# Performance work log

Hardware: AMD Instinct MI355X
Metric: run time of the kernel (lower is better)

Reference implementation:

```python
import jax, jax.numpy as jnp
import numpy as np

N = 10000      # nodes
E = 640000     # directed edges
D = 128        # feature width
C = 10         # classes
G = 64         # graphs in batch


def setup_inputs() -> dict:
    key = jax.random.key(0)
    ks = jax.random.split(key, 9)
    x = jax.random.normal(ks[0], (N, D), dtype=jnp.float32)
    edge_index = jax.random.randint(ks[1], (2, E), 0, N, dtype=jnp.int64)
    batch = jnp.sort(jax.random.randint(ks[2], (N,), 0, G, dtype=jnp.int64))
    scale = 1.0 / np.sqrt(D)
    W1 = jax.random.normal(ks[3], (D, D), dtype=jnp.float32) * scale
    W2 = jax.random.normal(ks[4], (D, D), dtype=jnp.float32) * scale
    W3 = jax.random.normal(ks[5], (D, D), dtype=jnp.float32) * scale
    W4 = jax.random.normal(ks[6], (D, D), dtype=jnp.float32) * scale
    fc_w = jax.random.normal(ks[7], (D, C), dtype=jnp.float32) * scale
    fc_b = jnp.zeros((C,), dtype=jnp.float32)
    return {"x": x, "edge_index": edge_index, "batch": batch,
            "W1": W1, "W2": W2, "W3": W3, "W4": W4,
            "fc_w": fc_w, "fc_b": fc_b}


def _gcn_conv(x, src, dst, deg_inv_sqrt, W):
    # GCNConv: h = x @ W; aggregate D^{-1/2}(A+I)D^{-1/2} h; then ReLU (activation).
    h = x @ W                                        # [N, D]
    norm = deg_inv_sqrt[src] * deg_inv_sqrt[dst]     # [E]
    msgs = h[src] * norm[:, None]                    # gather + scale
    agg = jax.ops.segment_sum(msgs, dst, num_segments=N)
    agg = agg + h * (deg_inv_sqrt * deg_inv_sqrt)[:, None]  # self-loop term
    return jax.nn.relu(agg)


def reference(x, edge_index, batch, W1, W2, W3, W4, fc_w, fc_b):
    src, dst = edge_index[0], edge_index[1]
    # degree counting self-loops (A + I normalization)
    deg = jax.ops.segment_sum(jnp.ones((E,), x.dtype), dst, num_segments=N) + 1.0
    deg_inv_sqrt = jax.lax.rsqrt(deg)
    for W in (W1, W2, W3, W4):
        x = _gcn_conv(x, src, dst, deg_inv_sqrt, W)
    xr = jax.ops.segment_sum(x, batch, num_segments=G)   # global_add_pool
    logits = x @ fc_w + fc_b
    return jax.nn.log_softmax(logits, axis=1), xr
```

## Files before the change

### kernel.cpp

```cpp
#include <hip/hip_runtime.h>
#include <hip/hip_fp16.h>
#include <math.h>

#define N_NODES 10000
#define N_EDGES 640000
#define DIM     128
#define NCLS    10
#define NGRAPH  64
#define NB      157
#define BCAP    4608
#define EPB     4000
#define NPB     8

typedef unsigned int uint32;
typedef unsigned short ushort16;
typedef _Float16 h2v __attribute__((ext_vector_type(2)));

#define SEL_LO 0x00003C00u
#define SEL_HI 0x3C000000u

__device__ __forceinline__ h2v as_h2(uint32 u) { h2v r; __builtin_memcpy(&r, &u, 4); return r; }

__device__ __forceinline__ float fd2(uint32 w, uint32 p, float acc) {
#if __has_builtin(__builtin_amdgcn_fdot2)
    return __builtin_amdgcn_fdot2(as_h2(w), as_h2(p), acc, false);
#else
    h2v a = as_h2(w), b = as_h2(p);
    return acc + (float)a[0] * (float)b[0] + (float)a[1] * (float)b[1];
#endif
}
__device__ __forceinline__ float f16lo(uint32 u) { return (float)as_h2(u)[0]; }
__device__ __forceinline__ float f16hi(uint32 u) { return (float)as_h2(u)[1]; }
__device__ __forceinline__ ushort16 f32_f16(float f) {
    return __half_as_ushort(__float2half(f));
}
__device__ __forceinline__ uint32 pack_f16x2(float lo, float hi) {
    __half2 h = __floats2half2_rn(lo, hi);
    uint32 u; __builtin_memcpy(&u, &h, 4); return u;
}

__global__ __launch_bounds__(256) void binA_gemm1(const int* __restrict__ src,
                                                  const int* __restrict__ dst,
                                                  int* __restrict__ gcursor,
                                                  uint32* __restrict__ bins,
                                                  const float* __restrict__ X,
                                                  const float* __restrict__ W,
                                                  const float* __restrict__ W2,
                                                  const float* __restrict__ W3,
                                                  const float* __restrict__ W4,
                                                  uint32* __restrict__ Wp,
                                                  ushort16* __restrict__ Gh,
                                                  float* __restrict__ xr) {
    __shared__ uint32 pk[EPB];
    __shared__ int cntS[NB], offS[NB], curS[NB], gposS[NB];

    if (blockIdx.x < 625) {
        int c    = threadIdx.x & 127;
        int rg   = threadIdx.x >> 7;
        int row0 = blockIdx.x * 16 + rg * 8;
        const float* xb = X + row0 * DIM;
        float acc[8] = {0.f, 0.f, 0.f, 0.f, 0.f, 0.f, 0.f, 0.f};
        for (int k = 0; k < DIM; k += 4) {
            float w0 = W[(k + 0) * DIM + c];
            float w1 = W[(k + 1) * DIM + c];
            float w2 = W[(k + 2) * DIM + c];
            float w3 = W[(k + 3) * DIM + c];
#pragma unroll
            for (int r = 0; r < 8; r++) {
                float4 xv = *(const float4*)(xb + r * DIM + k);
                acc[r] += xv.x * w0 + xv.y * w1 + xv.z * w2 + xv.w * w3;
            }
        }
#pragma unroll
        for (int r = 0; r < 8; r++)
            Gh[(row0 + r) * DIM + c] = f32_f16(acc[r]);
        return;
    }

    if (blockIdx.x >= 786) {
        int w = blockIdx.x - 786;
        const float* Ws = (w == 0) ? W2 : (w == 1) ? W3 : W4;
        uint32* Wd = Wp + w * (64 * DIM);
        for (int i = threadIdx.x; i < 64 * DIM; i += 256) {
            int k2 = i >> 7, c = i & 127;
            Wd[i] = pack_f16x2(Ws[(2 * k2) * DIM + c], Ws[(2 * k2 + 1) * DIM + c]);
        }
        return;
    }

    if (blockIdx.x == 785) {
        float4 z = make_float4(0.f, 0.f, 0.f, 0.f);
        for (int j = threadIdx.x; j < NGRAPH * DIM / 4; j += 256)
            ((float4*)xr)[j] = z;
        return;
    }

    int ab  = blockIdx.x - 625;
    int tid = threadIdx.x;
    for (int i = tid; i < NB; i += 256) cntS[i] = 0;
    __syncthreads();

    int base = ab * EPB;
    uint32 pr[16];
#pragma unroll
    for (int it = 0; it < 16; it++) {
        int i = it * 256 + tid;
        uint32 p = 0xffffffffu;
        if (i < EPB) {
            int e = base + i;
            p = ((uint32)dst[e] << 16) | (uint32)src[e];
            atomicAdd(&cntS[p >> 22], 1);
        }
        pr[it] = p;
    }
    __syncthreads();

    if (tid < 64) {
        int carry = 0;
        for (int r = 0; r < 3; r++) {
            int idx = r * 64 + tid;
            int v = (idx < NB) ? cntS[idx] : 0;
            int inc = v;
#pragma unroll
            for (int o = 1; o < 64; o <<= 1) {
                int u = __shfl_up(inc, o, 64);
                if (tid >= o) inc += u;
            }
            if (idx < NB) { offS[idx] = inc - v + carry; curS[idx] = inc - v + carry; }
            carry += __shfl(inc, 63, 64);
        }
    }
    __syncthreads();

#pragma unroll
    for (int it = 0; it < 16; it++) {
        uint32 p = pr[it];
        if (p != 0xffffffffu) {
            int b = p >> 22;
            pk[atomicAdd(&curS[b], 1)] = p;
        }
    }
    __syncthreads();

    if (tid < NB) gposS[tid] = atomicAdd(&gcursor[tid], cntS[tid]);
    __syncthreads();

#pragma unroll
    for (int it = 0; it < 16; it++) {
        int i = it * 256 + tid;
        if (i < EPB) {
            uint32 u = pk[i];
            int b = u >> 22;
            int gp = gposS[b] + (i - offS[b]);
            if (gp < BCAP) bins[b * BCAP + gp] = u;
        }
    }
}

__global__ __launch_bounds__(256) void binB2(const int* __restrict__ gcursor,
                                             const uint32* __restrict__ bins,
                                             ushort16* __restrict__ col,
                                             int* __restrict__ deg,
                                             float* __restrict__ dis,
                                             uint32* __restrict__ disPh) {
    __shared__ ushort16 adj[32 * 128];
    __shared__ int cnt2[32];
    int b    = blockIdx.x >> 1;
    int half = blockIdx.x & 1;
    int tid  = threadIdx.x;
    if (tid < 32) cnt2[tid] = 0;
    __syncthreads();
    int tc = gcursor[b];
    if (tc > BCAP) tc = BCAP;
    const uint32* bb = bins + b * BCAP;
    for (int i = tid; i < tc; i += 256) {
        uint32 u = bb[i];
        int local = (u >> 16) & 63;
        if ((local >> 5) == half) {
            int l5 = local & 31;
            int r = atomicAdd(&cnt2[l5], 1);
            if (r < 128) adj[(l5 << 7) + r] = (ushort16)(u & 0xffffu);
        }
    }
    __syncthreads();
    uint4* dstp = (uint4*)(col + (size_t)b * 64 * 128 + half * 32 * 128);
    const uint4* srcp = (const uint4*)adj;
    for (int j = tid; j < 512; j += 256) dstp[j] = srcp[j];
    if (tid < 32) {
        int node = b * 64 + half * 32 + tid;
        int c = cnt2[tid] < 128 ? cnt2[tid] : 128;
        float dv = rsqrtf((float)c + 1.0f);
        deg[node] = c;
        dis[node] = dv;
        disPh[node] = (uint32)__half_as_ushort(__float2half(dv));
    }
}

template <bool SCALED_IN, bool PACK_OUT>
__device__ __forceinline__ void agg_to_lds(const ushort16* __restrict__ Gh,
                                           const int* __restrict__ deg,
                                           const ushort16* __restrict__ col,
                                           const float* __restrict__ dis,
                                           const uint32* __restrict__ disPh,
                                           void* __restrict__ Xout) {
    int tid  = threadIdx.x;
    int wave = tid >> 6;
    int lane = tid & 63;
    int grp  = lane >> 4;
    int sl   = lane & 15;
    const uint32* g32 = (const uint32*)Gh;
    const uint32* gp  = g32 + (sl << 2);

#pragma unroll
    for (int i = 0; i < 2; i++) {
        int vr = wave * 2 + i;
        int v  = blockIdx.x * NPB + vr;
        int dv = deg[v];
        uint32 colpack = ((const uint32*)(col + ((size_t)v << 7)))[lane];
        float acc[8];
#pragma unroll
        for (int j = 0; j < 8; j++) acc[j] = 0.f;

        int kk = 0;
        for (; kk + 16 <= dv; kk += 16) {
            int k0 = kk + grp, k1 = kk + 4 + grp, k2 = kk + 8 + grp, k3 = kk + 12 + grp;
            uint32 cp0 = __shfl(colpack, k0 >> 1, 64);
            uint32 cp1 = __shfl(colpack, k1 >> 1, 64);
            uint32 cp2 = __shfl(colpack, k2 >> 1, 64);
            uint32 cp3 = __shfl(colpack, k3 >> 1, 64);
            int u0 = (k0 & 1) ? (int)(cp0 >> 16) : (int)(cp0 & 0xffffu);
            int u1 = (k1 & 1) ? (int)(cp1 >> 16) : (int)(cp1 & 0xffffu);
            int u2 = (k2 & 1) ? (int)(cp2 >> 16) : (int)(cp2 & 0xffffu);
            int u3 = (k3 & 1) ? (int)(cp3 >> 16) : (int)(cp3 & 0xffffu);
            uint4 w0 = *(const uint4*)(gp + (u0 << 6));
            uint4 w1 = *(const uint4*)(gp + (u1 << 6));
            uint4 w2 = *(const uint4*)(gp + (u2 << 6));
            uint4 w3 = *(const uint4*)(gp + (u3 << 6));
            if (SCALED_IN) {
                acc[0] = fd2(w0.x, SEL_LO, acc[0]); acc[1] = fd2(w0.x, SEL_HI, acc[1]);
                acc[2] = fd2(w0.y, SEL_LO, acc[2]); acc[3] = fd2(w0.y, SEL_HI, acc[3]);
                acc[4] = fd2(w0.z, SEL_LO, acc[4]); acc[5] = fd2(w0.z, SEL_HI, acc[5]);
                acc[6] = fd2(w0.w, SEL_LO, acc[6]); acc[7] = fd2(w0.w, SEL_HI, acc[7]);
                acc[0] = fd2(w1.x, SEL_LO, acc[0]); acc[1] = fd2(w1.x, SEL_HI, acc[1]);
                acc[2] = fd2(w1.y, SEL_LO, acc[2]); acc[3] = fd2(w1.y, SEL_HI, acc[3]);
                acc[4] = fd2(w1.z, SEL_LO, acc[4]); acc[5] = fd2(w1.z, SEL_HI, acc[5]);
                acc[6] = fd2(w1.w, SEL_LO, acc[6]); acc[7] = fd2(w1.w, SEL_HI, acc[7]);
                acc[0] = fd2(w2.x, SEL_LO, acc[0]); acc[1] = fd2(w2.x, SEL_HI, acc[1]);
                acc[2] = fd2(w2.y, SEL_LO, acc[2]); acc[3] = fd2(w2.y, SEL_HI, acc[3]);
                acc[4] = fd2(w2.z, SEL_LO, acc[4]); acc[5] = fd2(w2.z, SEL_HI, acc[5]);
                acc[6] = fd2(w2.w, SEL_LO, acc[6]); acc[7] = fd2(w2.w, SEL_HI, acc[7]);
                acc[0] = fd2(w3.x, SEL_LO, acc[0]); acc[1] = fd2(w3.x, SEL_HI, acc[1]);
                acc[2] = fd2(w3.y, SEL_LO, acc[2]); acc[3] = fd2(w3.y, SEL_HI, acc[3]);
                acc[4] = fd2(w3.z, SEL_LO, acc[4]); acc[5] = fd2(w3.z, SEL_HI, acc[5]);
                acc[6] = fd2(w3.w, SEL_LO, acc[6]); acc[7] = fd2(w3.w, SEL_HI, acc[7]);
            } else {
                uint32 dp0 = disPh[u0], dp1 = disPh[u1], dp2 = disPh[u2], dp3 = disPh[u3];
                uint32 dq0 = dp0 << 16, dq1 = dp1 << 16, dq2 = dp2 << 16, dq3 = dp3 << 16;
                acc[0] = fd2(w0.x, dp0, acc[0]); acc[1] = fd2(w0.x, dq0, acc[1]);
                acc[2] = fd2(w0.y, dp0, acc[2]); acc[3] = fd2(w0.y, dq0, acc[3]);
                acc[4] = fd2(w0.z, dp0, acc[4]); acc[5] = fd2(w0.z, dq0, acc[5]);
                acc[6] = fd2(w0.w, dp0, acc[6]); acc[7] = fd2(w0.w, dq0, acc[7]);
                acc[0] = fd2(w1.x, dp1, acc[0]); acc[1] = fd2(w1.x, dq1, acc[1]);
                acc[2] = fd2(w1.y, dp1, acc[2]); acc[3] = fd2(w1.y, dq1, acc[3]);
                acc[4] = fd2(w1.z, dp1, acc[4]); acc[5] = fd2(w1.z, dq1, acc[5]);
                acc[6] = fd2(w1.w, dp1, acc[6]); acc[7] = fd2(w1.w, dq1, acc[7]);
                acc[0] = fd2(w2.x, dp2, acc[0]); acc[1] = fd2(w2.x, dq2, acc[1]);
                acc[2] = fd2(w2.y, dp2, acc[2]); acc[3] = fd2(w2.y, dq2, acc[3]);
                acc[4] = fd2(w2.z, dp2, acc[4]); acc[5] = fd2(w2.z, dq2, acc[5]);
                acc[6] = fd2(w2.w, dp2, acc[6]); acc[7] = fd2(w2.w, dq2, acc[7]);
                acc[0] = fd2(w3.x, dp3, acc[0]); acc[1] = fd2(w3.x, dq3, acc[1]);
                acc[2] = fd2(w3.y, dp3, acc[2]); acc[3] = fd2(w3.y, dq3, acc[3]);
                acc[4] = fd2(w3.z, dp3, acc[4]); acc[5] = fd2(w3.z, dq3, acc[5]);
                acc[6] = fd2(w3.w, dp3, acc[6]); acc[7] = fd2(w3.w, dq3, acc[7]);
            }
        }
        for (; kk + 8 <= dv; kk += 8) {
            int k0 = kk + grp, k1 = kk + 4 + grp;
            uint32 cp0 = __shfl(colpack, k0 >> 1, 64);
            uint32 cp1 = __shfl(colpack, k1 >> 1, 64);
            int u0 = (k0 & 1) ? (int)(cp0 >> 16) : (int)(cp0 & 0xffffu);
            int u1 = (k1 & 1) ? (int)(cp1 >> 16) : (int)(cp1 & 0xffffu);
            uint4 w0 = *(const uint4*)(gp + (u0 << 6));
            uint4 w1 = *(const uint4*)(gp + (u1 << 6));
            uint32 dp0 = SCALED_IN ? SEL_LO : disPh[u0];
            uint32 dp1 = SCALED_IN ? SEL_LO : disPh[u1];
            uint32 dq0 = SCALED_IN ? SEL_HI : (dp0 << 16);
            uint32 dq1 = SCALED_IN ? SEL_HI : (dp1 << 16);
            acc[0] = fd2(w0.x, dp0, acc[0]); acc[1] = fd2(w0.x, dq0, acc[1]);
            acc[2] = fd2(w0.y, dp0, acc[2]); acc[3] = fd2(w0.y, dq0, acc[3]);
            acc[4] = fd2(w0.z, dp0, acc[4]); acc[5] = fd2(w0.z, dq0, acc[5]);
            acc[6] = fd2(w0.w, dp0, acc[6]); acc[7] = fd2(w0.w, dq0, acc[7]);
            acc[0] = fd2(w1.x, dp1, acc[0]); acc[1] = fd2(w1.x, dq1, acc[1]);
            acc[2] = fd2(w1.y, dp1, acc[2]); acc[3] = fd2(w1.y, dq1, acc[3]);
            acc[4] = fd2(w1.z, dp1, acc[4]); acc[5] = fd2(w1.z, dq1, acc[5]);
            acc[6] = fd2(w1.w, dp1, acc[6]); acc[7] = fd2(w1.w, dq1, acc[7]);
        }
        for (; kk < dv; kk += 4) {
            int k = kk + grp;
            uint32 cp = __shfl(colpack, (k >> 1) & 63, 64);
            int u = (k & 1) ? (int)(cp >> 16) : (int)(cp & 0xffffu);
            if (k < dv) {
                uint4 w = *(const uint4*)(gp + (u << 6));
                uint32 dp = SCALED_IN ? SEL_LO : disPh[u];
                uint32 dq = SCALED_IN ? SEL_HI : (dp << 16);
                acc[0] = fd2(w.x, dp, acc[0]); acc[1] = fd2(w.x, dq, acc[1]);
                acc[2] = fd2(w.y, dp, acc[2]); acc[3] = fd2(w.y, dq, acc[3]);
                acc[4] = fd2(w.z, dp, acc[4]); acc[5] = fd2(w.z, dq, acc[5]);
                acc[6] = fd2(w.w, dp, acc[6]); acc[7] = fd2(w.w, dq, acc[7]);
            }
        }
#pragma unroll
        for (int j = 0; j < 8; j++) {
            acc[j] += __shfl_xor(acc[j], 16, 64);
            acc[j] += __shfl_xor(acc[j], 32, 64);
        }
        float sv = dis[v];
        uint4 hs = *(const uint4*)(gp + (v << 6));
        float fs = SCALED_IN ? 1.f : sv;
        float r0 = sv * (acc[0] + fs * f16lo(hs.x));
        float r1 = sv * (acc[1] + fs * f16hi(hs.x));
        float r2 = sv * (acc[2] + fs * f16lo(hs.y));
        float r3 = sv * (acc[3] + fs * f16hi(hs.y));
        float r4 = sv * (acc[4] + fs * f16lo(hs.z));
        float r5 = sv * (acc[5] + fs * f16hi(hs.z));
        float r6 = sv * (acc[6] + fs * f16lo(hs.w));
        float r7 = sv * (acc[7] + fs * f16hi(hs.w));
        if (grp == 0) {
            if (PACK_OUT) {
                uint32* o = (uint32*)Xout + vr * 64 + sl * 4;
                uint4 pk4;
                pk4.x = pack_f16x2(fmaxf(r0, 0.f), fmaxf(r1, 0.f));
                pk4.y = pack_f16x2(fmaxf(r2, 0.f), fmaxf(r3, 0.f));
                pk4.z = pack_f16x2(fmaxf(r4, 0.f), fmaxf(r5, 0.f));
                pk4.w = pack_f16x2(fmaxf(r6, 0.f), fmaxf(r7, 0.f));
                *(uint4*)o = pk4;
            } else {
                float4* o = (float4*)((float*)Xout + vr * DIM + sl * 8);
                o[0] = make_float4(fmaxf(r0, 0.f), fmaxf(r1, 0.f),
                                   fmaxf(r2, 0.f), fmaxf(r3, 0.f));
                o[1] = make_float4(fmaxf(r4, 0.f), fmaxf(r5, 0.f),
                                   fmaxf(r6, 0.f), fmaxf(r7, 0.f));
            }
        }
    }
}

template <bool SCALED_IN>
__global__ __launch_bounds__(256) void fused_layer(const ushort16* __restrict__ Gh_in,
                                                   const int* __restrict__ deg,
                                                   const ushort16* __restrict__ col,
                                                   const float* __restrict__ dis,
                                                   const uint32* __restrict__ disPh,
                                                   const uint32* __restrict__ Wp,
                                                   ushort16* __restrict__ Gh_out) {
    __shared__ __align__(16) uint32 Xh[NPB * 64];
    agg_to_lds<SCALED_IN, true>(Gh_in, deg, col, dis, disPh, Xh);
    __syncthreads();

    int c  = threadIdx.x & 127;
    int rg = threadIdx.x >> 7;
    int row0 = blockIdx.x * NPB + rg * 4;
    const uint4* Xh4 = (const uint4*)Xh;
    float acc[4] = {0.f, 0.f, 0.f, 0.f};
    for (int q = 0; q < 16; q++) {
        uint32 wp0 = Wp[(4 * q + 0) * DIM + c];
        uint32 wp1 = Wp[(4 * q + 1) * DIM + c];
        uint32 wp2 = Wp[(4 * q + 2) * DIM + c];
        uint32 wp3 = Wp[(4 * q + 3) * DIM + c];
#pragma unroll
        for (int r = 0; r < 4; r++) {
            uint4 xv = Xh4[(rg * 4 + r) * 16 + q];
            acc[r] = fd2(xv.x, wp0, acc[r]);
            acc[r] = fd2(xv.y, wp1, acc[r]);
            acc[r] = fd2(xv.z, wp2, acc[r]);
            acc[r] = fd2(xv.w, wp3, acc[r]);
        }
    }
#pragma unroll
    for (int r = 0; r < 4; r++) {
        int row = row0 + r;
        Gh_out[row * DIM + c] = f32_f16(acc[r] * dis[row]);
    }
}

__global__ __launch_bounds__(256) void fused_last(const ushort16* __restrict__ Gh_in,
                                                  const int* __restrict__ deg,
                                                  const ushort16* __restrict__ col,
                                                  const float* __restrict__ dis,
                                                  const uint32* __restrict__ disPh,
                                                  const int* __restrict__ batch,
                                                  const float* __restrict__ fcw,
                                                  const float* __restrict__ fcb,
                                                  float* __restrict__ xr,
                                                  float* __restrict__ out) {
    __shared__ float Xs[NPB * DIM];
    agg_to_lds<true, false>(Gh_in, deg, col, dis, disPh, Xs);
    __syncthreads();

    int wave = threadIdx.x >> 6;
    int lane = threadIdx.x & 63;
#pragma unroll
    for (int i = 0; i < 2; i++) {
        int vr   = wave * 2 + i;
        int node = blockIdx.x * NPB + vr;
        float xl = Xs[vr * DIM + lane];
        float xh = Xs[vr * DIM + 64 + lane];
        float lg[NCLS];
#pragma unroll
        for (int c2 = 0; c2 < NCLS; c2++) {
            float p = xl * fcw[lane * NCLS + c2] + xh * fcw[(lane + 64) * NCLS + c2];
#pragma unroll
            for (int off = 32; off >= 1; off >>= 1) p += __shfl_xor(p, off, 64);
            lg[c2] = p + fcb[c2];
        }
        float m = lg[0];
#pragma unroll
        for (int c2 = 1; c2 < NCLS; c2++) m = fmaxf(m, lg[c2]);
        float s = 0.f;
#pragma unroll
        for (int c2 = 0; c2 < NCLS; c2++) s += expf(lg[c2] - m);
        float lse = m + logf(s);
        if (lane < NCLS) out[node * NCLS + lane] = lg[lane] - lse;
    }

    if (threadIdx.x < 128) {
        int start = blockIdx.x * NPB;
        int t = threadIdx.x;
        int b = batch[start];
        float a = 0.f;
        for (int n = 0; n < NPB; n++) {
            int bn = batch[start + n];
            if (bn != b) { atomicAdd(&xr[b * DIM + t], a); a = 0.f; b = bn; }
            a += Xs[n * DIM + t];
        }
        atomicAdd(&xr[b * DIM + t], a);
    }
}


extern "C" void kernel_launch(void* const* d_in, const int* in_sizes, int n_in,
                              void* d_out, int out_size, void* d_ws, size_t ws_size,
                              hipStream_t stream) {
    const float* x     = (const float*)d_in[0];
    const int*   ei    = (const int*)d_in[1];
    const int*   src   = ei;
    const int*   dst   = ei + N_EDGES;
    const int*   batch = (const int*)d_in[2];
    const float* W1    = (const float*)d_in[3];
    const float* W2    = (const float*)d_in[4];
    const float* W3    = (const float*)d_in[5];
    const float* W4    = (const float*)d_in[6];
    const float* fcw   = (const float*)d_in[7];
    const float* fcb   = (const float*)d_in[8];

    float* out_ls = (float*)d_out;
    float* out_xr = out_ls + N_NODES * NCLS;

    int*      gcursor = (int*)d_ws;
    int*      deg     = gcursor + 256;
    float*    dis     = (float*)(deg + 10240);
    uint32*   bins    = (uint32*)(dis + 10240);
    ushort16* col     = (ushort16*)(bins + NB * BCAP);
    ushort16* Gh_a    = col + (size_t)NB * 64 * 128;
    ushort16* Gh_b    = Gh_a + (size_t)N_NODES * DIM;
    uint32*   Wp      = (uint32*)(Gh_b + (size_t)N_NODES * DIM);
    uint32*   disPh   = Wp + 3 * 64 * DIM;

    hipMemsetAsync(gcursor, 0, 256 * sizeof(int), stream);

    binA_gemm1<<<789, 256, 0, stream>>>(src, dst, gcursor, bins, x, W1,
                                        W2, W3, W4, Wp, Gh_a, out_xr);
    binB2     <<<2 * NB, 256, 0, stream>>>(gcursor, bins, col, deg, dis, disPh);

    fused_layer<false><<<N_NODES / NPB, 256, 0, stream>>>(Gh_a, deg, col, dis, disPh,
                                                          Wp, Gh_b);
    fused_layer<true> <<<N_NODES / NPB, 256, 0, stream>>>(Gh_b, deg, col, dis, disPh,
                                                          Wp + 64 * DIM, Gh_a);
    fused_layer<true> <<<N_NODES / NPB, 256, 0, stream>>>(Gh_a, deg, col, dis, disPh,
                                                          Wp + 2 * 64 * DIM, Gh_b);
    fused_last        <<<N_NODES / NPB, 256, 0, stream>>>(Gh_b, deg, col, dis, disPh,
                                                          batch, fcw, fcb, out_xr, out_ls);
}
```

Before: 182.2 us.

## Use fixed per-block bin segments and prescale first-layer features in binB2

Binning now writes each edge block's per-bucket entries into a fixed 64-slot segment with a per-segment count, instead of reserving space with global atomics on a cursor. This removes the memset and the cross-block atomic contention. binB2 also prescales the first layer's fp16 features by the source degree factor, so all layers share one aggregation path with no per-edge disPh gather. The cost is that binB2 scans a sparse 160x64 segment grid, and any segment holding more than 64 entries is silently truncated. That is unlikely with ~25 entries per segment on random inputs, but it is a correctness risk for skewed graphs.

New measurement: 190.4 us. 1.05x slower.

```diff
diff --git a/kernel.cpp b/kernel.cpp
--- a/kernel.cpp
+++ b/kernel.cpp
@@ -8,7 +8,8 @@
 #define NCLS    10
 #define NGRAPH  64
 #define NB      157
-#define BCAP    4608
+#define NBB     160
+#define SEG     64
 #define EPB     4000
 #define NPB     8
 
@@ -41,7 +42,7 @@
 
 __global__ __launch_bounds__(256) void binA_gemm1(const int* __restrict__ src,
                                                   const int* __restrict__ dst,
-                                                  int* __restrict__ gcursor,
+                                                  int* __restrict__ cntG,
                                                   uint32* __restrict__ bins,
                                                   const float* __restrict__ X,
                                                   const float* __restrict__ W,
@@ -52,7 +53,7 @@
                                                   ushort16* __restrict__ Gh,
                                                   float* __restrict__ xr) {
     __shared__ uint32 pk[EPB];
-    __shared__ int cntS[NB], offS[NB], curS[NB], gposS[NB];
+    __shared__ int cntS[NB], offS[NB], curS[NB];
 
     if (blockIdx.x < 625) {
         int c    = threadIdx.x & 127;
@@ -142,66 +143,84 @@
     }
     __syncthreads();
 
-    if (tid < NB) gposS[tid] = atomicAdd(&gcursor[tid], cntS[tid]);
-    __syncthreads();
-
 #pragma unroll
     for (int it = 0; it < 16; it++) {
         int i = it * 256 + tid;
         if (i < EPB) {
             uint32 u = pk[i];
             int b = u >> 22;
-            int gp = gposS[b] + (i - offS[b]);
-            if (gp < BCAP) bins[b * BCAP + gp] = u;
-        }
-    }
-}
-
-__global__ __launch_bounds__(256) void binB2(const int* __restrict__ gcursor,
+            int gp = i - offS[b];
+            if (gp < SEG) bins[(size_t)(b * NBB + ab) * SEG + gp] = u;
+        }
+    }
+    if (tid < NB) {
+        int c = cntS[tid];
+        cntG[tid * NBB + ab] = c < SEG ? c : SEG;
+    }
+}
+
+__global__ __launch_bounds__(256) void binB2(const int* __restrict__ cntG,
                                              const uint32* __restrict__ bins,
                                              ushort16* __restrict__ col,
                                              int* __restrict__ deg,
                                              float* __restrict__ dis,
-                                             uint32* __restrict__ disPh) {
+                                             ushort16* __restrict__ Gh) {
     __shared__ ushort16 adj[32 * 128];
     __shared__ int cnt2[32];
+    __shared__ int segc[NBB];
     int b    = blockIdx.x >> 1;
     int half = blockIdx.x & 1;
     int tid  = threadIdx.x;
     if (tid < 32) cnt2[tid] = 0;
-    __syncthreads();
-    int tc = gcursor[b];
-    if (tc > BCAP) tc = BCAP;
-    const uint32* bb = bins + b * BCAP;
-    for (int i = tid; i < tc; i += 256) {
-        uint32 u = bb[i];
-        int local = (u >> 16) & 63;
-        if ((local >> 5) == half) {
-            int l5 = local & 31;
-            int r = atomicAdd(&cnt2[l5], 1);
-            if (r < 128) adj[(l5 << 7) + r] = (ushort16)(u & 0xffffu);
-        }
-    }
-    __syncthreads();
+    if (tid < NBB) segc[tid] = cntG[b * NBB + tid];
+    __syncthreads();
+
+    const uint32* bb = bins + (size_t)b * NBB * SEG;
+    for (int i = tid; i < NBB * SEG; i += 256) {
+        int seg = i >> 6, idx = i & 63;
+        if (idx < segc[seg]) {
+            uint32 u = bb[i];
+            int local = (u >> 16) & 63;
+            if ((local >> 5) == half) {
+                int l5 = local & 31;
+                int r = atomicAdd(&cnt2[l5], 1);
+                if (r < 128) adj[(l5 << 7) + r] = (ushort16)(u & 0xffffu);
+            }
+        }
+    }
+    __syncthreads();
+
     uint4* dstp = (uint4*)(col + (size_t)b * 64 * 128 + half * 32 * 128);
     const uint4* srcp = (const uint4*)adj;
     for (int j = tid; j < 512; j += 256) dstp[j] = srcp[j];
     if (tid < 32) {
         int node = b * 64 + half * 32 + tid;
         int c = cnt2[tid] < 128 ? cnt2[tid] : 128;
+        deg[node] = c;
+        dis[node] = rsqrtf((float)c + 1.0f);
+    }
+
+    uint4* Gh4 = (uint4*)Gh;
+    int node0 = b * 64 + half * 32;
+    for (int j = tid; j < 32 * 16; j += 256) {
+        int rl = j >> 4, q = j & 15;
+        if (node0 + rl >= N_NODES) continue;
+        int c = cnt2[rl] < 128 ? cnt2[rl] : 128;
         float dv = rsqrtf((float)c + 1.0f);
-        deg[node] = c;
-        dis[node] = dv;
-        disPh[node] = (uint32)__half_as_ushort(__float2half(dv));
-    }
-}
-
-template <bool SCALED_IN, bool PACK_OUT>
+        uint4 g = Gh4[(size_t)(node0 + rl) * 16 + q];
+        g.x = pack_f16x2(f16lo(g.x) * dv, f16hi(g.x) * dv);
+        g.y = pack_f16x2(f16lo(g.y) * dv, f16hi(g.y) * dv);
+        g.z = pack_f16x2(f16lo(g.z) * dv, f16hi(g.z) * dv);
+        g.w = pack_f16x2(f16lo(g.w) * dv, f16hi(g.w) * dv);
+        Gh4[(size_t)(node0 + rl) * 16 + q] = g;
+    }
+}
+
+template <bool PACK_OUT>
 __device__ __forceinline__ void agg_to_lds(const ushort16* __restrict__ Gh,
                                            const int* __restrict__ deg,
                                            const ushort16* __restrict__ col,
                                            const float* __restrict__ dis,
-                                           const uint32* __restrict__ disPh,
                                            void* __restrict__ Xout) {
     int tid  = threadIdx.x;
     int wave = tid >> 6;
@@ -236,43 +255,22 @@
             uint4 w1 = *(const uint4*)(gp + (u1 << 6));
             uint4 w2 = *(const uint4*)(gp + (u2 << 6));
             uint4 w3 = *(const uint4*)(gp + (u3 << 6));
-            if (SCALED_IN) {
-                acc[0] = fd2(w0.x, SEL_LO, acc[0]); acc[1] = fd2(w0.x, SEL_HI, acc[1]);
-                acc[2] = fd2(w0.y, SEL_LO, acc[2]); acc[3] = fd2(w0.y, SEL_HI, acc[3]);
-                acc[4] = fd2(w0.z, SEL_LO, acc[4]); acc[5] = fd2(w0.z, SEL_HI, acc[5]);
-                acc[6] = fd2(w0.w, SEL_LO, acc[6]); acc[7] = fd2(w0.w, SEL_HI, acc[7]);
-                acc[0] = fd2(w1.x, SEL_LO, acc[0]); acc[1] = fd2(w1.x, SEL_HI, acc[1]);
-                acc[2] = fd2(w1.y, SEL_LO, acc[2]); acc[3] = fd2(w1.y, SEL_HI, acc[3]);
-                acc[4] = fd2(w1.z, SEL_LO, acc[4]); acc[5] = fd2(w1.z, SEL_HI, acc[5]);
-                acc[6] = fd2(w1.w, SEL_LO, acc[6]); acc[7] = fd2(w1.w, SEL_HI, acc[7]);
-                acc[0] = fd2(w2.x, SEL_LO, acc[0]); acc[1] = fd2(w2.x, SEL_HI, acc[1]);
-                acc[2] = fd2(w2.y, SEL_LO, acc[2]); acc[3] = fd2(w2.y, SEL_HI, acc[3]);
-                acc[4] = fd2(w2.z, SEL_LO, acc[4]); acc[5] = fd2(w2.z, SEL_HI, acc[5]);
-                acc[6] = fd2(w2.w, SEL_LO, acc[6]); acc[7] = fd2(w2.w, SEL_HI, acc[7]);
-                acc[0] = fd2(w3.x, SEL_LO, acc[0]); acc[1] = fd2(w3.x, SEL_HI, acc[1]);
-                acc[2] = fd2(w3.y, SEL_LO, acc[2]); acc[3] = fd2(w3.y, SEL_HI, acc[3]);
-                acc[4] = fd2(w3.z, SEL_LO, acc[4]); acc[5] = fd2(w3.z, SEL_HI, acc[5]);
-                acc[6] = fd2(w3.w, SEL_LO, acc[6]); acc[7] = fd2(w3.w, SEL_HI, acc[7]);
-            } else {
-                uint32 dp0 = disPh[u0], dp1 = disPh[u1], dp2 = disPh[u2], dp3 = disPh[u3];
-                uint32 dq0 = dp0 << 16, dq1 = dp1 << 16, dq2 = dp2 << 16, dq3 = dp3 << 16;
-                acc[0] = fd2(w0.x, dp0, acc[0]); acc[1] = fd2(w0.x, dq0, acc[1]);
-                acc[2] = fd2(w0.y, dp0, acc[2]); acc[3] = fd2(w0.y, dq0, acc[3]);
-                acc[4] = fd2(w0.z, dp0, acc[4]); acc[5] = fd2(w0.z, dq0, acc[5]);
-                acc[6] = fd2(w0.w, dp0, acc[6]); acc[7] = fd2(w0.w, dq0, acc[7]);
-                acc[0] = fd2(w1.x, dp1, acc[0]); acc[1] = fd2(w1.x, dq1, acc[1]);
-                acc[2] = fd2(w1.y, dp1, acc[2]); acc[3] = fd2(w1.y, dq1, acc[3]);
-                acc[4] = fd2(w1.z, dp1, acc[4]); acc[5] = fd2(w1.z, dq1, acc[5]);
-                acc[6] = fd2(w1.w, dp1, acc[6]); acc[7] = fd2(w1.w, dq1, acc[7]);
-                acc[0] = fd2(w2.x, dp2, acc[0]); acc[1] = fd2(w2.x, dq2, acc[1]);
-                acc[2] = fd2(w2.y, dp2, acc[2]); acc[3] = fd2(w2.y, dq2, acc[3]);
-                acc[4] = fd2(w2.z, dp2, acc[4]); acc[5] = fd2(w2.z, dq2, acc[5]);
-                acc[6] = fd2(w2.w, dp2, acc[6]); acc[7] = fd2(w2.w, dq2, acc[7]);
-                acc[0] = fd2(w3.x, dp3, acc[0]); acc[1] = fd2(w3.x, dq3, acc[1]);
-                acc[2] = fd2(w3.y, dp3, acc[2]); acc[3] = fd2(w3.y, dq3, acc[3]);
-                acc[4] = fd2(w3.z, dp3, acc[4]); acc[5] = fd2(w3.z, dq3, acc[5]);
-                acc[6] = fd2(w3.w, dp3, acc[6]); acc[7] = fd2(w3.w, dq3, acc[7]);
-            }
+            acc[0] = fd2(w0.x, SEL_LO, acc[0]); acc[1] = fd2(w0.x, SEL_HI, acc[1]);
+            acc[2] = fd2(w0.y, SEL_LO, acc[2]); acc[3] = fd2(w0.y, SEL_HI, acc[3]);
+            acc[4] = fd2(w0.z, SEL_LO, acc[4]); acc[5] = fd2(w0.z, SEL_HI, acc[5]);
+            acc[6] = fd2(w0.w, SEL_LO, acc[6]); acc[7] = fd2(w0.w, SEL_HI, acc[7]);
+            acc[0] = fd2(w1.x, SEL_LO, acc[0]); acc[1] = fd2(w1.x, SEL_HI, acc[1]);
+            acc[2] = fd2(w1.y, SEL_LO, acc[2]); acc[3] = fd2(w1.y, SEL_HI, acc[3]);
+            acc[4] = fd2(w1.z, SEL_LO, acc[4]); acc[5] = fd2(w1.z, SEL_HI, acc[5]);
+            acc[6] = fd2(w1.w, SEL_LO, acc[6]); acc[7] = fd2(w1.w, SEL_HI, acc[7]);
+            acc[0] = fd2(w2.x, SEL_LO, acc[0]); acc[1] = fd2(w2.x, SEL_HI, acc[1]);
+            acc[2] = fd2(w2.y, SEL_LO, acc[2]); acc[3] = fd2(w2.y, SEL_HI, acc[3]);
+            acc[4] = fd2(w2.z, SEL_LO, acc[4]); acc[5] = fd2(w2.z, SEL_HI, acc[5]);
+            acc[6] = fd2(w2.w, SEL_LO, acc[6]); acc[7] = fd2(w2.w, SEL_HI, acc[7]);
+            acc[0] = fd2(w3.x, SEL_LO, acc[0]); acc[1] = fd2(w3.x, SEL_HI, acc[1]);
+            acc[2] = fd2(w3.y, SEL_LO, acc[2]); acc[3] = fd2(w3.y, SEL_HI, acc[3]);
+            acc[4] = fd2(w3.z, SEL_LO, acc[4]); acc[5] = fd2(w3.z, SEL_HI, acc[5]);
+            acc[6] = fd2(w3.w, SEL_LO, acc[6]); acc[7] = fd2(w3.w, SEL_HI, acc[7]);
         }
         for (; kk + 8 <= dv; kk += 8) {
             int k0 = kk + grp, k1 = kk + 4 + grp;
@@ -282,18 +280,14 @@
             int u1 = (k1 & 1) ? (int)(cp1 >> 16) : (int)(cp1 & 0xffffu);
             uint4 w0 = *(const uint4*)(gp + (u0 << 6));
             uint4 w1 = *(const uint4*)(gp + (u1 << 6));
-            uint32 dp0 = SCALED_IN ? SEL_LO : disPh[u0];
-            uint32 dp1 = SCALED_IN ? SEL_LO : disPh[u1];
-            uint32 dq0 = SCALED_IN ? SEL_HI : (dp0 << 16);
-            uint32 dq1 = SCALED_IN ? SEL_HI : (dp1 << 16);
-            acc[0] = fd2(w0.x, dp0, acc[0]); acc[1] = fd2(w0.x, dq0, acc[1]);
-            acc[2] = fd2(w0.y, dp0, acc[2]); acc[3] = fd2(w0.y, dq0, acc[3]);
-            acc[4] = fd2(w0.z, dp0, acc[4]); acc[5] = fd2(w0.z, dq0, acc[5]);
-            acc[6] = fd2(w0.w, dp0, acc[6]); acc[7] = fd2(w0.w, dq0, acc[7]);
-            acc[0] = fd2(w1.x, dp1, acc[0]); acc[1] = fd2(w1.x, dq1, acc[1]);
-            acc[2] = fd2(w1.y, dp1, acc[2]); acc[3] = fd2(w1.y, dq1, acc[3]);
-            acc[4] = fd2(w1.z, dp1, acc[4]); acc[5] = fd2(w1.z, dq1, acc[5]);
-            acc[6] = fd2(w1.w, dp1, acc[6]); acc[7] = fd2(w1.w, dq1, acc[7]);
+            acc[0] = fd2(w0.x, SEL_LO, acc[0]); acc[1] = fd2(w0.x, SEL_HI, acc[1]);
+            acc[2] = fd2(w0.y, SEL_LO, acc[2]); acc[3] = fd2(w0.y, SEL_HI, acc[3]);
+            acc[4] = fd2(w0.z, SEL_LO, acc[4]); acc[5] = fd2(w0.z, SEL_HI, acc[5]);
+            acc[6] = fd2(w0.w, SEL_LO, acc[6]); acc[7] = fd2(w0.w, SEL_HI, acc[7]);
+            acc[0] = fd2(w1.x, SEL_LO, acc[0]); acc[1] = fd2(w1.x, SEL_HI, acc[1]);
+            acc[2] = fd2(w1.y, SEL_LO, acc[2]); acc[3] = fd2(w1.y, SEL_HI, acc[3]);
+            acc[4] = fd2(w1.z, SEL_LO, acc[4]); acc[5] = fd2(w1.z, SEL_HI, acc[5]);
+            acc[6] = fd2(w1.w, SEL_LO, acc[6]); acc[7] = fd2(w1.w, SEL_HI, acc[7]);
         }
         for (; kk < dv; kk += 4) {
             int k = kk + grp;
@@ -301,12 +295,10 @@
             int u = (k & 1) ? (int)(cp >> 16) : (int)(cp & 0xffffu);
             if (k < dv) {
                 uint4 w = *(const uint4*)(gp + (u << 6));
-                uint32 dp = SCALED_IN ? SEL_LO : disPh[u];
-                uint32 dq = SCALED_IN ? SEL_HI : (dp << 16);
-                acc[0] = fd2(w.x, dp, acc[0]); acc[1] = fd2(w.x, dq, acc[1]);
-                acc[2] = fd2(w.y, dp, acc[2]); acc[3] = fd2(w.y, dq, acc[3]);
-                acc[4] = fd2(w.z, dp, acc[4]); acc[5] = fd2(w.z, dq, acc[5]);
-                acc[6] = fd2(w.w, dp, acc[6]); acc[7] = fd2(w.w, dq, acc[7]);
+                acc[0] = fd2(w.x, SEL_LO, acc[0]); acc[1] = fd2(w.x, SEL_HI, acc[1]);
+                acc[2] = fd2(w.y, SEL_LO, acc[2]); acc[3] = fd2(w.y, SEL_HI, acc[3]);
+                acc[4] = fd2(w.z, SEL_LO, acc[4]); acc[5] = fd2(w.z, SEL_HI, acc[5]);
+                acc[6] = fd2(w.w, SEL_LO, acc[6]); acc[7] = fd2(w.w, SEL_HI, acc[7]);
             }
         }
 #pragma unroll
@@ -316,15 +308,14 @@
         }
         float sv = dis[v];
         uint4 hs = *(const uint4*)(gp + (v << 6));
-        float fs = SCALED_IN ? 1.f : sv;
-        float r0 = sv * (acc[0] + fs * f16lo(hs.x));
-        float r1 = sv * (acc[1] + fs * f16hi(hs.x));
-        float r2 = sv * (acc[2] + fs * f16lo(hs.y));
-        float r3 = sv * (acc[3] + fs * f16hi(hs.y));
-        float r4 = sv * (acc[4] + fs * f16lo(hs.z));
-        float r5 = sv * (acc[5] + fs * f16hi(hs.z));
-        float r6 = sv * (acc[6] + fs * f16lo(hs.w));
-        float r7 = sv * (acc[7] + fs * f16hi(hs.w));
+        float r0 = sv * (acc[0] + f16lo(hs.x));
+        float r1 = sv * (acc[1] + f16hi(hs.x));
+        float r2 = sv * (acc[2] + f16lo(hs.y));
+        float r3 = sv * (acc[3] + f16hi(hs.y));
+        float r4 = sv * (acc[4] + f16lo(hs.z));
+        float r5 = sv * (acc[5] + f16hi(hs.z));
+        float r6 = sv * (acc[6] + f16lo(hs.w));
+        float r7 = sv * (acc[7] + f16hi(hs.w));
         if (grp == 0) {
             if (PACK_OUT) {
                 uint32* o = (uint32*)Xout + vr * 64 + sl * 4;
@@ -345,16 +336,14 @@
     }
 }
 
-template <bool SCALED_IN>
 __global__ __launch_bounds__(256) void fused_layer(const ushort16* __restrict__ Gh_in,
                                                    const int* __restrict__ deg,
                                                    const ushort16* __restrict__ col,
                                                    const float* __restrict__ dis,
-                                                   const uint32* __restrict__ disPh,
                                                    const uint32* __restrict__ Wp,
                                                    ushort16* __restrict__ Gh_out) {
     __shared__ __align__(16) uint32 Xh[NPB * 64];
-    agg_to_lds<SCALED_IN, true>(Gh_in, deg, col, dis, disPh, Xh);
+    agg_to_lds<true>(Gh_in, deg, col, dis, Xh);
     __syncthreads();
 
     int c  = threadIdx.x & 127;
@@ -387,14 +376,13 @@
                                                   const int* __restrict__ deg,
                                                   const ushort16* __restrict__ col,
                                                   const float* __restrict__ dis,
-                                                  const uint32* __restrict__ disPh,
                                                   const int* __restrict__ batch,
                                                   const float* __restrict__ fcw,
                                                   const float* __restrict__ fcb,
                                                   float* __restrict__ xr,
                                                   float* __restrict__ out) {
     __shared__ float Xs[NPB * DIM];
-    agg_to_lds<true, false>(Gh_in, deg, col, dis, disPh, Xs);
+    agg_to_lds<false>(Gh_in, deg, col, dis, Xs);
     __syncthreads();
 
     int wave = threadIdx.x >> 6;
@@ -456,28 +444,24 @@
     float* out_ls = (float*)d_out;
     float* out_xr = out_ls + N_NODES * NCLS;
 
-    int*      gcursor = (int*)d_ws;
-    int*      deg     = gcursor + 256;
-    float*    dis     = (float*)(deg + 10240);
-    uint32*   bins    = (uint32*)(dis + 10240);
-    ushort16* col     = (ushort16*)(bins + NB * BCAP);
-    ushort16* Gh_a    = col + (size_t)NB * 64 * 128;
-    ushort16* Gh_b    = Gh_a + (size_t)N_NODES * DIM;
-    uint32*   Wp      = (uint32*)(Gh_b + (size_t)N_NODES * DIM);
-    uint32*   disPh   = Wp + 3 * 64 * DIM;
-
-    hipMemsetAsync(gcursor, 0, 256 * sizeof(int), stream);
-
-    binA_gemm1<<<789, 256, 0, stream>>>(src, dst, gcursor, bins, x, W1,
+    int*      cntG = (int*)d_ws;
+    int*      deg  = cntG + NB * NBB;
+    float*    dis  = (float*)(deg + 10240);
+    uint32*   bins = (uint32*)(dis + 10240);
+    ushort16* col  = (ushort16*)(bins + (size_t)NB * NBB * SEG);
+    ushort16* Gh_a = col + (size_t)NB * 64 * 128;
+    ushort16* Gh_b = Gh_a + (size_t)N_NODES * DIM;
+    uint32*   Wp   = (uint32*)(Gh_b + (size_t)N_NODES * DIM);
+
+    binA_gemm1<<<789, 256, 0, stream>>>(src, dst, cntG, bins, x, W1,
                                         W2, W3, W4, Wp, Gh_a, out_xr);
-    binB2     <<<2 * NB, 256, 0, stream>>>(gcursor, bins, col, deg, dis, disPh);
-
-    fused_layer<false><<<N_NODES / NPB, 256, 0, stream>>>(Gh_a, deg, col, dis, disPh,
-                                                          Wp, Gh_b);
-    fused_layer<true> <<<N_NODES / NPB, 256, 0, stream>>>(Gh_b, deg, col, dis, disPh,
-                                                          Wp + 64 * DIM, Gh_a);
-    fused_layer<true> <<<N_NODES / NPB, 256, 0, stream>>>(Gh_a, deg, col, dis, disPh,
-                                                          Wp + 2 * 64 * DIM, Gh_b);
-    fused_last        <<<N_NODES / NPB, 256, 0, stream>>>(Gh_b, deg, col, dis, disPh,
-                                                          batch, fcw, fcb, out_xr, out_ls);
-}
+    binB2     <<<2 * NB, 256, 0, stream>>>(cntG, bins, col, deg, dis, Gh_a);
+
+    fused_layer<<<N_NODES / NPB, 256, 0, stream>>>(Gh_a, deg, col, dis, Wp, Gh_b);
+    fused_layer<<<N_NODES / NPB, 256, 0, stream>>>(Gh_b, deg, col, dis,
+                                                   Wp + 64 * DIM, Gh_a);
+    fused_layer<<<N_NODES / NPB, 256, 0, stream>>>(Gh_a, deg, col, dis,
+                                                   Wp + 2 * 64 * DIM, Gh_b);
+    fused_last <<<N_NODES / NPB, 256, 0, stream>>>(Gh_b, deg, col, dis, batch,
+                                                   fcw, fcb, out_xr, out_ls);
+}
```
